# Performance work log

Measured on AMD Instinct MI355X. Metric: run time of the kernel, lower is better.

## Reference

```python
import jax, jax.numpy as jnp
import numpy as np

N_CLUSTERS = 8
ENC_IN = 862
SEQ_LEN = 720
PRED_LEN = 336
BATCH = 64


def setup_inputs() -> dict:
    key = jax.random.key(0)
    k1, k2, k3, k4 = jax.random.split(key, 4)
    x = jax.random.normal(k1, (BATCH, ENC_IN, SEQ_LEN), dtype=jnp.float32)
    clusters = jax.random.randint(k2, (ENC_IN,), 0, N_CLUSTERS, dtype=jnp.int64)
    # Per-cluster Linear(seq_len -> pred_len): weight [P, S], bias [P], like nn.Linear
    bound = 1.0 / np.sqrt(SEQ_LEN)
    W = jax.random.uniform(k3, (N_CLUSTERS, PRED_LEN, SEQ_LEN), dtype=jnp.float32, minval=-bound, maxval=bound)
    b = jax.random.uniform(k4, (N_CLUSTERS, PRED_LEN), dtype=jnp.float32, minval=-bound, maxval=bound)
    return {"x": x, "clusters": clusters, "W": W, "b": b}


def reference(x, clusters, W, b):
    # Gather each channel's cluster weight/bias, then batched per-channel GEMV.
    Wc = W[clusters]            # [C, P, S]
    bc = b[clusters]            # [C, P]
    # out[b, c, p] = sum_s x[b, c, s] * Wc[c, p, s] + bc[c, p]
    out = jnp.einsum('bcs,cps->bcp', x, Wc) + bc[None, :, :]
    return out
```

## Files before the change

### kernel.cpp

```cpp
#include <hip/hip_runtime.h>
#include <stdint.h>

#define N_CL    8
#define C_IN    862
#define SEQ     720
#define SEQP    768
#define PRED    336
#define BATCH   64
#define BK      32
#define NCHUNK  23
#define NT      (PRED / 16)
#define XBSTRIDE ((size_t)C_IN * SEQ)

#define BROWS   384
#define BBYTES  (BROWS * 64)
#define NBISS   24

typedef __attribute__((ext_vector_type(8))) __bf16 bf16x8;
typedef __attribute__((ext_vector_type(4))) float  floatx4;

__device__ __forceinline__ void async16(const void* g, void* l) {
  __builtin_amdgcn_global_load_lds(
      (__attribute__((address_space(1))) unsigned int*)(uintptr_t)g,
      (__attribute__((address_space(3))) unsigned int*)l,
      16, 0, 0);
}

__global__ void wconv_kernel(const float* __restrict__ W, __bf16* __restrict__ Wb) {
  const int row = blockIdx.x;
  const float* src = W + (size_t)row * SEQ;
  __bf16* dst = Wb + (size_t)row * SEQP;
  for (int s = threadIdx.x; s < SEQP; s += blockDim.x) {
    float v = (s < SEQ) ? src[s] : 0.0f;
    dst[s] = (__bf16)v;
  }
}

__global__ __launch_bounds__(256, 3) void clin_kernel(
    const float* __restrict__ x, const int* __restrict__ clusters,
    const __bf16* __restrict__ Wb, const float* __restrict__ bias,
    float* __restrict__ out) {
  __shared__ __attribute__((aligned(128))) unsigned char smem[2 * BBYTES];

  const int c    = blockIdx.x;
  const int cl   = clusters[c];
  const int tid  = threadIdx.x;
  const int wave = tid >> 6;
  const int lane = tid & 63;
  const int q    = lane >> 4;
  const int ln   = lane & 15;

  const int mrow  = (wave << 4) + ln;
  const int klane = q << 3;

  const float*  xr = x  + (size_t)mrow * XBSTRIDE + (size_t)c * SEQ + klane;
  const __bf16* wc = Wb + (size_t)cl * PRED * SEQP;

  const int srow  = lane >> 2;
  const int sgran = (lane & 3) ^ ((lane >> 2) & 3);
  const int brd = ln * 64 + (((q ^ (ln & 3)) & 3) << 4);

  floatx4 acc[NT];
#pragma unroll
  for (int t = 0; t < NT; ++t) acc[t] = (floatx4){0.f, 0.f, 0.f, 0.f};

#define STAGE_B(k0, Bdst)                                                    \
  {                                                                          \
    _Pragma("unroll")                                                        \
    for (int i = wave; i < NBISS; i += 4) {                                  \
      int r  = (i << 4) + srow;                                              \
      int rs = (r < PRED) ? r : 0;     \
      async16(wc + (size_t)rs * SEQP + (k0) + (sgran << 3), (Bdst) + i * 1024); \
    }                                                                        \
  }

#define LOAD_A(k0, f0, f1)                                                   \
  {                                                                          \
    const float* ap = ((k0) + klane < SEQ) ? (xr + (k0)) : xr;               \
    f0 = *(const floatx4*)ap;                                                \
    f1 = *(const floatx4*)(ap + 4);                                          \
  }

#define COMPUTE(Bsrc, f0, f1)                                                \
  {                                                                          \
    bf16x8 a;                                                                \
    a[0] = (__bf16)f0[0]; a[1] = (__bf16)f0[1];                              \
    a[2] = (__bf16)f0[2]; a[3] = (__bf16)f0[3];                              \
    a[4] = (__bf16)f1[0]; a[5] = (__bf16)f1[1];                              \
    a[6] = (__bf16)f1[2]; a[7] = (__bf16)f1[3];                              \
    _Pragma("unroll")                                                        \
    for (int tt = 0; tt < NT; ++tt) {                                        \
      bf16x8 b = *(const bf16x8*)((Bsrc) + tt * 1024 + brd);                 \
      acc[tt] = __builtin_amdgcn_mfma_f32_16x16x32_bf16(a, b, acc[tt], 0, 0, 0); \
    }                                                                        \
  }

  unsigned char* const Bbuf0 = smem;
  unsigned char* const Bbuf1 = smem + BBYTES;

  floatx4 a0c, a1c, a0n, a1n;

  STAGE_B(0, Bbuf0);
  LOAD_A(0, a0c, a1c);

#pragma unroll 2
  for (int t = 0; t < NCHUNK - 1; ++t) {
    unsigned char* Bc = (t & 1) ? Bbuf1 : Bbuf0;
    unsigned char* Bn = (t & 1) ? Bbuf0 : Bbuf1;
    const int k0n = (t + 1) * BK;

    STAGE_B(k0n, Bn);
    LOAD_A(k0n, a0n, a1n);

    asm volatile("s_waitcnt vmcnt(8)" ::: "memory");
    __builtin_amdgcn_s_barrier();

    COMPUTE(Bc, a0c, a1c);

    __builtin_amdgcn_s_barrier();
    a0c = a0n; a1c = a1n;
  }

  asm volatile("s_waitcnt vmcnt(0)" ::: "memory");
  __builtin_amdgcn_s_barrier();
  {
    unsigned char* Bc = ((NCHUNK - 1) & 1) ? Bbuf1 : Bbuf0;
    COMPUTE(Bc, a0c, a1c);
  }

  const float* bc = bias + cl * PRED;
#pragma unroll
  for (int t = 0; t < NT; ++t) {
    int p = (t << 4) + ln;
    float bv = bc[p];
#pragma unroll
    for (int r = 0; r < 4; ++r) {
      int brow = (wave << 4) + (q << 2) + r;
      out[((size_t)brow * C_IN + c) * PRED + p] = acc[t][r] + bv;
    }
  }
#undef STAGE_B
#undef LOAD_A
#undef COMPUTE
}

extern "C" void kernel_launch(void* const* d_in, const int* in_sizes, int n_in,
                              void* d_out, int out_size, void* d_ws, size_t ws_size,
                              hipStream_t stream) {
  const float* x   = (const float*)d_in[0];
  const int*   cls = (const int*)d_in[1];
  const float* W   = (const float*)d_in[2];
  const float* b   = (const float*)d_in[3];
  float* out = (float*)d_out;
  __bf16* Wb = (__bf16*)d_ws;

  hipLaunchKernelGGL(wconv_kernel, dim3(N_CL * PRED), dim3(256), 0, stream, W, Wb);
  hipLaunchKernelGGL(clin_kernel, dim3(C_IN), dim3(256), 0, stream,
                     x, cls, Wb, b, out);
}
```

Before: 314.2 us.

## Prefetch A two chunks ahead and repack B LDS tiles with 128-byte rows

Changes the LDS layout of the staged weight tile to 128-byte physical rows holding two 16-row groups, with a new XOR swizzle for staging and reads. Fully unrolls the K loop and uses indexed A register arrays so x loads are issued two chunks ahead instead of one, with a looser vmcnt wait. The aim is to hide global latency on the x stream and reduce LDS bank conflicts, at the cost of more registers, which could hurt occupancy under the 3-blocks launch bound.

```diff
diff --git a/kernel.cpp b/kernel.cpp
--- a/kernel.cpp
+++ b/kernel.cpp
@@ -12,8 +12,8 @@
 #define NT      (PRED / 16)
 #define XBSTRIDE ((size_t)C_IN * SEQ)
 
-#define BROWS   384
-#define BBYTES  (BROWS * 64)
+#define PHYSR   192
+#define BBYTES  (PHYSR * 128)
 #define NBISS   24
 
 typedef __attribute__((ext_vector_type(8))) __bf16 bf16x8;
@@ -56,76 +56,84 @@
   const float*  xr = x  + (size_t)mrow * XBSTRIDE + (size_t)c * SEQ + klane;
   const __bf16* wc = Wb + (size_t)cl * PRED * SEQP;
 
-  const int srow  = lane >> 2;
-  const int sgran = (lane & 3) ^ ((lane >> 2) & 3);
-  const int brd = ln * 64 + (((q ^ (ln & 3)) & 3) << 4);
+  const int s_c2   = (lane & 7) ^ (lane >> 3);
+  const int s_g    = s_c2 & 3;
+  const int s_nb   = (lane >> 3) + 192 * (s_c2 >> 2);
+
+  const int e    = ln & 7;
+  const int brd0 = ln * 128 + (((q    ) ^ e) << 4);
+  const int brd1 = ln * 128 + (((q + 4) ^ e) << 4) - 24576;
 
   floatx4 acc[NT];
 #pragma unroll
   for (int t = 0; t < NT; ++t) acc[t] = (floatx4){0.f, 0.f, 0.f, 0.f};
 
-#define STAGE_B(k0, Bdst)                                                    \
-  {                                                                          \
-    _Pragma("unroll")                                                        \
-    for (int i = wave; i < NBISS; i += 4) {                                  \
-      int r  = (i << 4) + srow;                                              \
-      int rs = (r < PRED) ? r : 0;     \
-      async16(wc + (size_t)rs * SEQP + (k0) + (sgran << 3), (Bdst) + i * 1024); \
-    }                                                                        \
+#define STAGE_B(k0, Bdst)                                                     \
+  {                                                                           \
+    _Pragma("unroll")                                                         \
+    for (int i = wave; i < NBISS; i += 4) {                                   \
+      int n  = (i << 3) + s_nb;                                               \
+      int ns = (n < PRED) ? n : 0;   \
+      async16(wc + (size_t)ns * SEQP + (k0) + (s_g << 3), (Bdst) + i * 1024); \
+    }                                                                         \
   }
 
-#define LOAD_A(k0, f0, f1)                                                   \
-  {                                                                          \
-    const float* ap = ((k0) + klane < SEQ) ? (xr + (k0)) : xr;               \
-    f0 = *(const floatx4*)ap;                                                \
-    f1 = *(const floatx4*)(ap + 4);                                          \
+#define LOAD_A(k0, f0, f1)                                                    \
+  {                                                                           \
+    const float* ap = ((k0) + klane < SEQ) ? (xr + (k0)) : xr;                \
+    f0 = *(const floatx4*)ap;                                                 \
+    f1 = *(const floatx4*)(ap + 4);                                           \
   }
 
-#define COMPUTE(Bsrc, f0, f1)                                                \
-  {                                                                          \
-    bf16x8 a;                                                                \
-    a[0] = (__bf16)f0[0]; a[1] = (__bf16)f0[1];                              \
-    a[2] = (__bf16)f0[2]; a[3] = (__bf16)f0[3];                              \
-    a[4] = (__bf16)f1[0]; a[5] = (__bf16)f1[1];                              \
-    a[6] = (__bf16)f1[2]; a[7] = (__bf16)f1[3];                              \
-    _Pragma("unroll")                                                        \
-    for (int tt = 0; tt < NT; ++tt) {                                        \
-      bf16x8 b = *(const bf16x8*)((Bsrc) + tt * 1024 + brd);                 \
+#define COMPUTE(Bsrc, f0, f1)                                                 \
+  {                                                                           \
+    bf16x8 a;                                                                 \
+    a[0] = (__bf16)f0[0]; a[1] = (__bf16)f0[1];                               \
+    a[2] = (__bf16)f0[2]; a[3] = (__bf16)f0[3];                               \
+    a[4] = (__bf16)f1[0]; a[5] = (__bf16)f1[1];                               \
+    a[6] = (__bf16)f1[2]; a[7] = (__bf16)f1[3];                               \
+    _Pragma("unroll")                                                         \
+    for (int tt = 0; tt < NT; ++tt) {                                         \
+      int off = tt * 2048 + (tt < 12 ? brd0 : brd1);                          \
+      bf16x8 b = *(const bf16x8*)((Bsrc) + off);                              \
       acc[tt] = __builtin_amdgcn_mfma_f32_16x16x32_bf16(a, b, acc[tt], 0, 0, 0); \
-    }                                                                        \
+    }                                                                         \
   }
 
-  unsigned char* const Bbuf0 = smem;
-  unsigned char* const Bbuf1 = smem + BBYTES;
+  unsigned char* const B0 = smem;
+  unsigned char* const B1 = smem + BBYTES;
 
-  floatx4 a0c, a1c, a0n, a1n;
+  floatx4 a0[NCHUNK + 2], a1[NCHUNK + 2];
 
-  STAGE_B(0, Bbuf0);
-  LOAD_A(0, a0c, a1c);
+  STAGE_B(0, B0);
+  __builtin_amdgcn_sched_barrier(0);
+  LOAD_A(0, a0[0], a1[0]);
+  LOAD_A(BK, a0[1], a1[1]);
+  __builtin_amdgcn_sched_barrier(0);
 
-#pragma unroll 2
+#pragma unroll
   for (int t = 0; t < NCHUNK - 1; ++t) {
-    unsigned char* Bc = (t & 1) ? Bbuf1 : Bbuf0;
-    unsigned char* Bn = (t & 1) ? Bbuf0 : Bbuf1;
-    const int k0n = (t + 1) * BK;
+    unsigned char* Bc = (t & 1) ? B1 : B0;
+    unsigned char* Bn = (t & 1) ? B0 : B1;
 
-    STAGE_B(k0n, Bn);
-    LOAD_A(k0n, a0n, a1n);
+    STAGE_B((t + 1) * BK, Bn);
+    __builtin_amdgcn_sched_barrier(0);
+    LOAD_A((t + 2) * BK, a0[t + 2], a1[t + 2]);
+    __builtin_amdgcn_sched_barrier(0);
 
-    asm volatile("s_waitcnt vmcnt(8)" ::: "memory");
+    asm volatile("s_waitcnt vmcnt(10)" ::: "memory");
     __builtin_amdgcn_s_barrier();
 
-    COMPUTE(Bc, a0c, a1c);
+    COMPUTE(Bc, a0[t], a1[t]);
 
     __builtin_amdgcn_s_barrier();
-    a0c = a0n; a1c = a1n;
   }
 
   asm volatile("s_waitcnt vmcnt(0)" ::: "memory");
   __builtin_amdgcn_s_barrier();
   {
-    unsigned char* Bc = ((NCHUNK - 1) & 1) ? Bbuf1 : Bbuf0;
-    COMPUTE(Bc, a0c, a1c);
+    unsigned char* Bc = ((NCHUNK - 1) & 1) ? B1 : B0;
+    COMPUTE(Bc, a0[NCHUNK - 1], a1[NCHUNK - 1]);
   }
 
   const float* bc = bias + cl * PRED;
```

Result: slower. 359.4 us (+14.4%).
